# Kernel tuning notes

Measured on AMD Instinct MI355X. Metric: run time of the kernel, lower is better.

Reference implementation:

```python
import jax, jax.numpy as jnp
import numpy as np

B, L, IN_DIM, OUT_DIM, N_BRANCH = 16, 1024, 300, 100, 60

def setup_inputs() -> dict:
    key = jax.random.key(0)
    ks = jax.random.split(key, 7)
    s = 0.05  # weight init scale
    return {
        "x": jax.random.normal(ks[0], (B, L, IN_DIM), dtype=jnp.float32),
        "W2": jax.random.normal(ks[1], (N_BRANCH, OUT_DIM, IN_DIM, 2), dtype=jnp.float32) * s,
        "b2": jax.random.normal(ks[2], (N_BRANCH, OUT_DIM), dtype=jnp.float32) * s,
        "W3": jax.random.normal(ks[3], (N_BRANCH, OUT_DIM, IN_DIM, 3), dtype=jnp.float32) * s,
        "b3": jax.random.normal(ks[4], (N_BRANCH, OUT_DIM), dtype=jnp.float32) * s,
        "W4": jax.random.normal(ks[5], (N_BRANCH, OUT_DIM, IN_DIM, 4), dtype=jnp.float32) * s,
        "b4": jax.random.normal(ks[6], (N_BRANCH, OUT_DIM), dtype=jnp.float32) * s,
    }

def _branch_group(xc, W, b):
    # xc: [B, C, L]; W: [n, o, c, k]; b: [n, o]
    # Batch all n same-kernel-size branches into ONE conv with n*o output channels.
    n, o, c, k = W.shape
    Wf = W.reshape(n * o, c, k)
    y = jax.lax.conv_general_dilated(
        xc, Wf, window_strides=(1,), padding="VALID",
        dimension_numbers=("NCH", "OIH", "NCH"))  # [B, n*o, L-k+1]
    y = jax.nn.relu(y + b.reshape(n * o)[None, :, None])
    y = jnp.max(y, axis=-1)                      # AdaptiveMaxPool1d(1): [B, n*o]
    # concat dim=2 in torch stacks branches along the length axis -> [B, o, n]
    return jnp.transpose(y.reshape(xc.shape[0], n, o), (0, 2, 1))

def reference(x, W2, b2, W3, b3, W4, b4):
    xc = jnp.transpose(x, (0, 2, 1))  # [B, in_dim, L]
    out = jnp.concatenate([
        _branch_group(xc, W2, b2),
        _branch_group(xc, W3, b3),
        _branch_group(xc, W4, b4),
    ], axis=2)                        # [B, out_dim, 180]
    # nn.Dropout(0.5) is identity in eval mode; omitted for the reference baseline.
    return out
```

## Files before the change

### kernel.cpp

```cpp
#include <hip/hip_runtime.h>
#include <cstdint>
#include <cstddef>

typedef unsigned short u16;
typedef unsigned int   u32;
typedef __attribute__((ext_vector_type(8))) short bf16x8;
typedef __attribute__((ext_vector_type(4))) float f32x4;

#define NB   16
#define LL   1024
#define CIN  300
#define CINP 320
#define XPBP (LL*CINP)
#define XELP (NB*XPBP)
#define NCH  6000
#define NCHP 6144
#define ODIM 100

#define BM 256
#define BN 256
#define BK 64

__device__ __forceinline__ u16 f2bf(float f) {
  union { float f; u32 u; } v; v.f = f;
  return (u16)((v.u + 0x7FFFu + ((v.u >> 16) & 1u)) >> 16);
}

typedef __attribute__((address_space(1))) const unsigned int gu32;
typedef __attribute__((address_space(3))) unsigned int lu32;
__device__ __forceinline__ void gload_lds16(const void* g, void* l) {
  __builtin_amdgcn_global_load_lds((gu32*)g, (lu32*)l, 16, 0, 0);
}

#define BAR() asm volatile("s_barrier" ::: "memory")
#define VM2  asm volatile("s_waitcnt vmcnt(2)" ::: "memory")
#define VM0  asm volatile("s_waitcnt vmcnt(0)" ::: "memory")

__global__ void cvt_x_kernel(const float* __restrict__ x, u16* __restrict__ xb) {
  int i8 = (blockIdx.x * 256 + threadIdx.x) * 8;
  int row = i8 / CINP;
  int col = i8 - row * CINP;
  const float* src = x + (size_t)row * CIN + col;
  u16 e[8];
  if (col + 8 <= CIN) {
    float4 a = *(const float4*)src;
    float4 b = *(const float4*)(src + 4);
    e[0]=f2bf(a.x); e[1]=f2bf(a.y); e[2]=f2bf(a.z); e[3]=f2bf(a.w);
    e[4]=f2bf(b.x); e[5]=f2bf(b.y); e[6]=f2bf(b.z); e[7]=f2bf(b.w);
  } else {
    #pragma unroll
    for (int j = 0; j < 8; j++)
      e[j] = (col + j < CIN) ? f2bf(src[j]) : (u16)0;
  }
  uint4 o;
  o.x = (u32)e[0] | ((u32)e[1] << 16);
  o.y = (u32)e[2] | ((u32)e[3] << 16);
  o.z = (u32)e[4] | ((u32)e[5] << 16);
  o.w = (u32)e[6] | ((u32)e[7] << 16);
  *(uint4*)(xb + i8) = o;
}

__global__ void repack_w_kernel(const float* __restrict__ W2, const float* __restrict__ W3,
                                const float* __restrict__ W4, u16* __restrict__ wb) {
  int g = blockIdx.y;
  int kk = g + 2;
  int Kp = kk * CINP;
  int woff = (g == 0) ? 0 : (g == 1) ? NCHP*640 : NCHP*(640+960);
  const float* W = (g == 0) ? W2 : (g == 1) ? W3 : W4;
  int no = blockIdx.x;
  u16* dst = wb + (size_t)woff + (size_t)no * Kp;
  const float* src = W + (size_t)no * (CIN * kk);
  for (int kp = threadIdx.x; kp < Kp; kp += 256) {
    int j = kp / CINP, c = kp - j * CINP;
    u16 v = 0;
    if (no < NCH && c < CIN) v = f2bf(src[c * kk + j]);
    dst[kp] = v;
  }
}

__global__ __launch_bounds__(512, 1)
void gemm_max_kernel(const u16* __restrict__ xb, const u16* __restrict__ wb,
                     const float* __restrict__ b2v, const float* __restrict__ b3v,
                     const float* __restrict__ b4v, float* __restrict__ out) {
  const int id    = blockIdx.x;
  const int g     = 2 - (id / 384);
  const int id2   = id % 384;
  const int b     = id2 / 24;
  const int chblk = id2 % 24;
  const int Kp    = (g + 2) * CINP;
  const int nks   = Kp >> 6;
  const int woff  = (g == 0) ? 0 : (g == 1) ? NCHP*640 : NCHP*(640+960);
  const int Lt    = LL - (g + 2) + 1;

  __shared__ __align__(16) u16 smem[4 * 16384];
  u16* A0s = smem;
  u16* B0s = smem + 16384;
  u16* A1s = smem + 32768;
  u16* B1s = smem + 49152;

  const int tid  = threadIdx.x;
  const int lane = tid & 63;
  const int w    = tid >> 6;
  const int wr   = w >> 2;
  const int wc   = w & 3;

  const u16* __restrict__ xrow = xb + (size_t)b * XPBP;
  const u16* __restrict__ Wg   = wb + (size_t)woff + (size_t)chblk * BN * Kp;

  auto STAGE = [&](const u16* src, int stride, u16* buf, int half) {
    #pragma unroll
    for (int i = 0; i < 2; i++) {
      int c = i * 512 + w * 64 + lane;
      int row128 = c >> 3;
      int colb = ((c & 7) * 16) ^ ((row128 & 7) << 4);
      gload_lds16(src + (size_t)(half * 128 + row128) * stride + (colb >> 1),
                  buf + half * 8192 + i * 4096 + w * 512);
    }
  };

  auto FR = [&](const u16* buf, int grp, int k) -> bf16x8 {
    int row  = grp * 16 + (lane & 15);
    int colb = (k * 64 + ((lane >> 4) << 4)) ^ ((lane & 7) << 4);
    return *(const bf16x8*)(buf + row * 64 + (colb >> 1));
  };

  f32x4 acc[8][4];
  #pragma unroll
  for (int mi = 0; mi < 8; mi++)
    #pragma unroll
    for (int ni = 0; ni < 4; ni++)
      acc[mi][ni] = (f32x4){0.f, 0.f, 0.f, 0.f};

  bf16x8 afrA[4][2];
  bf16x8 afrB[4][2];
  bf16x8 bfr[2][2][2];
  float rmax[4] = { -1e30f, -1e30f, -1e30f, -1e30f };

  auto FOLD = [&](int ttf) {
    #pragma unroll
    for (int mi = 0; mi < 8; mi++) {
      int tb = ttf * 256 + (mi * 2 + wr) * 16 + ((lane >> 4) << 2);
      #pragma unroll
      for (int r = 0; r < 4; r++) {
        bool ok = (tb + r) < Lt;
        #pragma unroll
        for (int ni = 0; ni < 4; ni++)
          if (ok) rmax[ni] = fmaxf(rmax[ni], acc[mi][ni][r]);
      }
      #pragma unroll
      for (int ni = 0; ni < 4; ni++)
        acc[mi][ni] = (f32x4){0.f, 0.f, 0.f, 0.f};
    }
  };

#define READ_A(DST, BUF, MH) do {                                             \
    _Pragma("unroll")                                                         \
    for (int a2 = 0; a2 < 4; a2++) {                                          \
      _Pragma("unroll")                                                       \
      for (int k2 = 0; k2 < 2; k2++)                                          \
        DST[a2][k2] = FR(BUF, ((MH)*4 + a2) * 2 + wr, k2);                    \
    }                                                                         \
  } while (0)

#define READ_B(NH, BUF) do {                                                  \
    _Pragma("unroll")                                                         \
    for (int b2 = 0; b2 < 2; b2++) {                                          \
      _Pragma("unroll")                                                       \
      for (int k2 = 0; k2 < 2; k2++)                                          \
        bfr[NH][b2][k2] = FR(BUF, ((NH)*2 + b2) * 4 + wc, k2);                \
    }                                                                         \
  } while (0)

#define MFMAQ(MH, NH, A) do {                                                 \
    __builtin_amdgcn_s_setprio(1);                                            \
    _Pragma("unroll")                                                         \
    for (int a2 = 0; a2 < 4; a2++)                                            \
      _Pragma("unroll")                                                       \
      for (int b2 = 0; b2 < 2; b2++)                                          \
        _Pragma("unroll")                                                     \
        for (int k2 = 0; k2 < 2; k2++)                                        \
          acc[(MH)*4 + a2][(NH)*2 + b2] =                                     \
            __builtin_amdgcn_mfma_f32_16x16x32_bf16(A[a2][k2],                \
              bfr[NH][b2][k2], acc[(MH)*4 + a2][(NH)*2 + b2], 0, 0, 0);       \
    __builtin_amdgcn_s_setprio(0);                                            \
  } while (0)

  const int NT = 4 * nks;
  int tt = 0, ks = 0;

  STAGE(xrow, CINP, A0s, 0);
  STAGE(Wg,   Kp,   B0s, 0);
  STAGE(Wg,   Kp,   B0s, 1);
  STAGE(xrow, CINP, A0s, 1);
  VM2;
  BAR();
  READ_A(afrA, A0s, 0);
  READ_B(0, B0s);

  for (int s = 0; s < NT - 1; s++) {
    int ks2 = ks + 1, tt2 = tt;
    if (ks2 == nks) { ks2 = 0; tt2++; }
    const u16* sA = xrow + (size_t)tt2 * (256 * CINP) + ks2 * 64;
    const u16* sB = Wg + ks2 * 64;
    u16* cA = (s & 1) ? A1s : A0s;
    u16* cB = (s & 1) ? B1s : B0s;
    u16* nA = (s & 1) ? A0s : A1s;
    u16* nB = (s & 1) ? B0s : B1s;

    STAGE(sA, CINP, nA, 0);
    BAR();
    MFMAQ(0, 0, afrA);
    VM2;
    READ_B(1, cB);
    BAR();
    STAGE(sB, Kp, nB, 0);
    BAR();
    MFMAQ(0, 1, afrA);
    READ_A(afrB, cA, 1);
    BAR();
    STAGE(sB, Kp, nB, 1);
    BAR();
    MFMAQ(1, 0, afrB);
    VM2;
    BAR();
    STAGE(sA, CINP, nA, 1);
    BAR();
    MFMAQ(1, 1, afrB);
    VM2;
    READ_A(afrA, nA, 0);
    READ_B(0, nB);
    BAR();

    if (++ks == nks) { FOLD(tt); ks = 0; tt++; }
  }

  {
    MFMAQ(0, 0, afrA);
    VM0;
    READ_B(1, B1s);
    BAR();
    MFMAQ(0, 1, afrA);
    READ_A(afrB, A1s, 1);
    MFMAQ(1, 0, afrB);
    MFMAQ(1, 1, afrB);
    FOLD(tt);
  }
#undef READ_A
#undef READ_B
#undef MFMAQ

  float cv[4];
  #pragma unroll
  for (int ni = 0; ni < 4; ni++) {
    float v = rmax[ni];
    v = fmaxf(v, __shfl_xor(v, 16));
    v = fmaxf(v, __shfl_xor(v, 32));
    cv[ni] = v;
  }
  __syncthreads();
  float* red = (float*)smem;
  if (lane < 16) {
    #pragma unroll
    for (int ni = 0; ni < 4; ni++)
      red[wr * 256 + (ni * 4 + wc) * 16 + lane] = cv[ni];
  }
  __syncthreads();
  const float* bias = (g == 0) ? b2v : (g == 1) ? b3v : b4v;
  if (tid < 256) {
    float v = fmaxf(red[tid], red[256 + tid]);
    int ch = chblk * BN + tid;
    if (ch < NCH) {
      int n = ch / ODIM, o = ch - n * ODIM;
      out[b * (ODIM * 180) + o * 180 + g * 60 + n] = fmaxf(v + bias[ch], 0.f);
    }
  }
}

extern "C" void kernel_launch(void* const* d_in, const int* in_sizes, int n_in,
                              void* d_out, int out_size, void* d_ws, size_t ws_size,
                              hipStream_t stream) {
  const float* x  = (const float*)d_in[0];
  const float* W2 = (const float*)d_in[1];
  const float* b2 = (const float*)d_in[2];
  const float* W3 = (const float*)d_in[3];
  const float* b3 = (const float*)d_in[4];
  const float* W4 = (const float*)d_in[5];
  const float* b4 = (const float*)d_in[6];
  float* out = (float*)d_out;

  u16* xb = (u16*)d_ws;
  u16* wb = xb + XELP;

  cvt_x_kernel<<<XELP / (256 * 8), 256, 0, stream>>>(x, xb);
  repack_w_kernel<<<dim3(NCHP, 3), 256, 0, stream>>>(W2, W3, W4, wb);
  gemm_max_kernel<<<dim3(1152), 512, 0, stream>>>(xb, wb, b2, b3, b4, out);
}
```

Before: 537.5 us.

## Switch GEMM to 32x32x16 MFMA tiles and merge prep kernels

Replaces the 16x16x32 bf16 MFMA tiling with 32x32x16 MFMA instructions, reorganizing fragment reads, accumulators (f32x16), the max-fold row mapping and the cross-lane reduction. Larger MFMA tiles reduce LDS fragment reads per flop and issue fewer instructions. It also fuses the x conversion and weight repack into a single launch to cut one kernel launch. Register pressure and the fold indexing change, so the row mapping must match the 32x32 output layout.

```diff
diff --git a/kernel.cpp b/kernel.cpp
--- a/kernel.cpp
+++ b/kernel.cpp
@@ -4,8 +4,8 @@
 
 typedef unsigned short u16;
 typedef unsigned int   u32;
-typedef __attribute__((ext_vector_type(8))) short bf16x8;
-typedef __attribute__((ext_vector_type(4))) float f32x4;
+typedef __attribute__((ext_vector_type(8)))  short bf16x8;
+typedef __attribute__((ext_vector_type(16))) float f32x16;
 
 #define NB   16
 #define LL   1024
@@ -36,45 +36,48 @@
 #define VM2  asm volatile("s_waitcnt vmcnt(2)" ::: "memory")
 #define VM0  asm volatile("s_waitcnt vmcnt(0)" ::: "memory")
 
-__global__ void cvt_x_kernel(const float* __restrict__ x, u16* __restrict__ xb) {
-  int i8 = (blockIdx.x * 256 + threadIdx.x) * 8;
-  int row = i8 / CINP;
-  int col = i8 - row * CINP;
-  const float* src = x + (size_t)row * CIN + col;
-  u16 e[8];
-  if (col + 8 <= CIN) {
-    float4 a = *(const float4*)src;
-    float4 b = *(const float4*)(src + 4);
-    e[0]=f2bf(a.x); e[1]=f2bf(a.y); e[2]=f2bf(a.z); e[3]=f2bf(a.w);
-    e[4]=f2bf(b.x); e[5]=f2bf(b.y); e[6]=f2bf(b.z); e[7]=f2bf(b.w);
+__global__ void prep_kernel(const float* __restrict__ x,
+                            const float* __restrict__ W2, const float* __restrict__ W3,
+                            const float* __restrict__ W4,
+                            u16* __restrict__ xb, u16* __restrict__ wb) {
+  int bid = blockIdx.x;
+  if (bid < 3 * NCHP) {
+    int g  = bid / NCHP;
+    int no = bid - g * NCHP;
+    int kk = g + 2;
+    int Kp = kk * CINP;
+    int woff = (g == 0) ? 0 : (g == 1) ? NCHP*640 : NCHP*(640+960);
+    const float* W = (g == 0) ? W2 : (g == 1) ? W3 : W4;
+    u16* dst = wb + (size_t)woff + (size_t)no * Kp;
+    const float* src = W + (size_t)no * (CIN * kk);
+    for (int kp = threadIdx.x; kp < Kp; kp += 256) {
+      int j = kp / CINP, c = kp - j * CINP;
+      u16 v = 0;
+      if (no < NCH && c < CIN) v = f2bf(src[c * kk + j]);
+      dst[kp] = v;
+    }
   } else {
-    #pragma unroll
-    for (int j = 0; j < 8; j++)
-      e[j] = (col + j < CIN) ? f2bf(src[j]) : (u16)0;
-  }
-  uint4 o;
-  o.x = (u32)e[0] | ((u32)e[1] << 16);
-  o.y = (u32)e[2] | ((u32)e[3] << 16);
-  o.z = (u32)e[4] | ((u32)e[5] << 16);
-  o.w = (u32)e[6] | ((u32)e[7] << 16);
-  *(uint4*)(xb + i8) = o;
-}
-
-__global__ void repack_w_kernel(const float* __restrict__ W2, const float* __restrict__ W3,
-                                const float* __restrict__ W4, u16* __restrict__ wb) {
-  int g = blockIdx.y;
-  int kk = g + 2;
-  int Kp = kk * CINP;
-  int woff = (g == 0) ? 0 : (g == 1) ? NCHP*640 : NCHP*(640+960);
-  const float* W = (g == 0) ? W2 : (g == 1) ? W3 : W4;
-  int no = blockIdx.x;
-  u16* dst = wb + (size_t)woff + (size_t)no * Kp;
-  const float* src = W + (size_t)no * (CIN * kk);
-  for (int kp = threadIdx.x; kp < Kp; kp += 256) {
-    int j = kp / CINP, c = kp - j * CINP;
-    u16 v = 0;
-    if (no < NCH && c < CIN) v = f2bf(src[c * kk + j]);
-    dst[kp] = v;
+    int i8 = ((bid - 3 * NCHP) * 256 + threadIdx.x) * 8;
+    int row = i8 / CINP;
+    int col = i8 - row * CINP;
+    const float* src = x + (size_t)row * CIN + col;
+    u16 e[8];
+    if (col + 8 <= CIN) {
+      float4 a = *(const float4*)src;
+      float4 b = *(const float4*)(src + 4);
+      e[0]=f2bf(a.x); e[1]=f2bf(a.y); e[2]=f2bf(a.z); e[3]=f2bf(a.w);
+      e[4]=f2bf(b.x); e[5]=f2bf(b.y); e[6]=f2bf(b.z); e[7]=f2bf(b.w);
+    } else {
+      #pragma unroll
+      for (int j = 0; j < 8; j++)
+        e[j] = (col + j < CIN) ? f2bf(src[j]) : (u16)0;
+    }
+    uint4 o;
+    o.x = (u32)e[0] | ((u32)e[1] << 16);
+    o.y = (u32)e[2] | ((u32)e[3] << 16);
+    o.z = (u32)e[4] | ((u32)e[5] << 16);
+    o.w = (u32)e[6] | ((u32)e[7] << 16);
+    *(uint4*)(xb + i8) = o;
   }
 }
 
@@ -118,70 +121,67 @@
     }
   };
 
-  auto FR = [&](const u16* buf, int grp, int k) -> bf16x8 {
-    int row  = grp * 16 + (lane & 15);
-    int colb = (k * 64 + ((lane >> 4) << 4)) ^ ((lane & 7) << 4);
+  auto FR32 = [&](const u16* buf, int grp, int ksl) -> bf16x8 {
+    int row  = grp * 32 + (lane & 31);
+    int colb = (ksl * 32 + ((lane >> 5) << 4)) ^ ((lane & 7) << 4);
     return *(const bf16x8*)(buf + row * 64 + (colb >> 1));
   };
 
-  f32x4 acc[8][4];
+  f32x16 acc[4][2];
   #pragma unroll
-  for (int mi = 0; mi < 8; mi++)
-    #pragma unroll
-    for (int ni = 0; ni < 4; ni++)
-      acc[mi][ni] = (f32x4){0.f, 0.f, 0.f, 0.f};
-
-  bf16x8 afrA[4][2];
-  bf16x8 afrB[4][2];
-  bf16x8 bfr[2][2][2];
-  float rmax[4] = { -1e30f, -1e30f, -1e30f, -1e30f };
+  for (int a2 = 0; a2 < 4; a2++)
+    #pragma unroll
+    for (int b2 = 0; b2 < 2; b2++)
+      #pragma unroll
+      for (int q = 0; q < 16; q++)
+        acc[a2][b2][q] = 0.f;
+
+  bf16x8 afrA[2][4];
+  bf16x8 afrB[2][4];
+  bf16x8 bfr[2][4];
+  float rmax[2] = { -1e30f, -1e30f };
 
   auto FOLD = [&](int ttf) {
     #pragma unroll
-    for (int mi = 0; mi < 8; mi++) {
-      int tb = ttf * 256 + (mi * 2 + wr) * 16 + ((lane >> 4) << 2);
+    for (int a2 = 0; a2 < 4; a2++) {
+      int rowbase = ttf * 256 + (a2 * 2 + wr) * 32 + ((lane >> 5) << 2);
       #pragma unroll
-      for (int r = 0; r < 4; r++) {
-        bool ok = (tb + r) < Lt;
+      for (int r = 0; r < 16; r++) {
+        int t = rowbase + (r & 3) + 8 * (r >> 2);
+        bool ok = t < Lt;
         #pragma unroll
-        for (int ni = 0; ni < 4; ni++)
-          if (ok) rmax[ni] = fmaxf(rmax[ni], acc[mi][ni][r]);
+        for (int b2 = 0; b2 < 2; b2++) {
+          if (ok) rmax[b2] = fmaxf(rmax[b2], acc[a2][b2][r]);
+          acc[a2][b2][r] = 0.f;
+        }
       }
-      #pragma unroll
-      for (int ni = 0; ni < 4; ni++)
-        acc[mi][ni] = (f32x4){0.f, 0.f, 0.f, 0.f};
     }
   };
 
-#define READ_A(DST, BUF, MH) do {                                             \
+#define READ_A32(DST, BUF, MH) do {                                           \
     _Pragma("unroll")                                                         \
-    for (int a2 = 0; a2 < 4; a2++) {                                          \
+    for (int a2l = 0; a2l < 2; a2l++) {                                       \
       _Pragma("unroll")                                                       \
-      for (int k2 = 0; k2 < 2; k2++)                                          \
-        DST[a2][k2] = FR(BUF, ((MH)*4 + a2) * 2 + wr, k2);                    \
+      for (int ksl = 0; ksl < 4; ksl++)                                       \
+        DST[a2l][ksl] = FR32(BUF, ((MH)*2 + a2l) * 2 + wr, ksl);              \
     }                                                                         \
   } while (0)
 
-#define READ_B(NH, BUF) do {                                                  \
+#define READ_B32(NH, BUF) do {                                                \
     _Pragma("unroll")                                                         \
-    for (int b2 = 0; b2 < 2; b2++) {                                          \
-      _Pragma("unroll")                                                       \
-      for (int k2 = 0; k2 < 2; k2++)                                          \
-        bfr[NH][b2][k2] = FR(BUF, ((NH)*2 + b2) * 4 + wc, k2);                \
-    }                                                                         \
+    for (int ksl = 0; ksl < 4; ksl++)                                         \
+      bfr[NH][ksl] = FR32(BUF, (NH)*4 + wc, ksl);                             \
   } while (0)
 
-#define MFMAQ(MH, NH, A) do {                                                 \
+#define MFMAQ32(MH, NH, A) do {                                               \
     __builtin_amdgcn_s_setprio(1);                                            \
     _Pragma("unroll")                                                         \
-    for (int a2 = 0; a2 < 4; a2++)                                            \
+    for (int ksl = 0; ksl < 4; ksl++)                                         \
       _Pragma("unroll")                                                       \
-      for (int b2 = 0; b2 < 2; b2++)                                          \
-        _Pragma("unroll")                                                     \
-        for (int k2 = 0; k2 < 2; k2++)                                        \
-          acc[(MH)*4 + a2][(NH)*2 + b2] =                                     \
-            __builtin_amdgcn_mfma_f32_16x16x32_bf16(A[a2][k2],                \
-              bfr[NH][b2][k2], acc[(MH)*4 + a2][(NH)*2 + b2], 0, 0, 0);       \
+      for (int a2l = 0; a2l < 2; a2l++)                                       \
+        acc[(MH)*2 + a2l][NH] =                                               \
+          __builtin_amdgcn_mfma_f32_32x32x16_bf16(A[a2l][ksl],                \
+            bfr[NH][ksl], acc[(MH)*2 + a2l][NH], 0, 0, 0);                    \
     __builtin_amdgcn_s_setprio(0);                                            \
   } while (0)
 
@@ -194,8 +194,8 @@
   STAGE(xrow, CINP, A0s, 1);
   VM2;
   BAR();
-  READ_A(afrA, A0s, 0);
-  READ_B(0, B0s);
+  READ_A32(afrA, A0s, 0);
+  READ_B32(0, B0s);
 
   for (int s = 0; s < NT - 1; s++) {
     int ks2 = ks + 1, tt2 = tt;
@@ -209,60 +209,59 @@
 
     STAGE(sA, CINP, nA, 0);
     BAR();
-    MFMAQ(0, 0, afrA);
+    MFMAQ32(0, 0, afrA);
     VM2;
-    READ_B(1, cB);
+    READ_B32(1, cB);
     BAR();
     STAGE(sB, Kp, nB, 0);
     BAR();
-    MFMAQ(0, 1, afrA);
-    READ_A(afrB, cA, 1);
+    MFMAQ32(0, 1, afrA);
+    READ_A32(afrB, cA, 1);
     BAR();
     STAGE(sB, Kp, nB, 1);
     BAR();
-    MFMAQ(1, 0, afrB);
+    MFMAQ32(1, 0, afrB);
     VM2;
     BAR();
     STAGE(sA, CINP, nA, 1);
     BAR();
-    MFMAQ(1, 1, afrB);
+    MFMAQ32(1, 1, afrB);
     VM2;
-    READ_A(afrA, nA, 0);
-    READ_B(0, nB);
+    READ_A32(afrA, nA, 0);
+    READ_B32(0, nB);
     BAR();
 
     if (++ks == nks) { FOLD(tt); ks = 0; tt++; }
   }
 
   {
-    MFMAQ(0, 0, afrA);
+    MFMAQ32(0, 0, afrA);
     VM0;
-    READ_B(1, B1s);
-    BAR();
-    MFMAQ(0, 1, afrA);
-    READ_A(afrB, A1s, 1);
-    MFMAQ(1, 0, afrB);
-    MFMAQ(1, 1, afrB);
+    READ_B32(1, B1s);
+    BAR();
+    MFMAQ32(0, 1, afrA);
+    READ_A32(afrB, A1s, 1);
+    MFMAQ32(1, 0, afrB);
+    MFMAQ32(1, 1, afrB);
     FOLD(tt);
   }
-#undef READ_A
-#undef READ_B
-#undef MFMAQ
-
-  float cv[4];
+#undef READ_A32
+#undef READ_B32
+#undef MFMAQ32
+
+  float cv[2];
   #pragma unroll
-  for (int ni = 0; ni < 4; ni++) {
-    float v = rmax[ni];
-    v = fmaxf(v, __shfl_xor(v, 16));
+  for (int b2 = 0; b2 < 2; b2++) {
+    float v = rmax[b2];
     v = fmaxf(v, __shfl_xor(v, 32));
-    cv[ni] = v;
+    cv[b2] = v;
   }
   __syncthreads();
   float* red = (float*)smem;
-  if (lane < 16) {
-    #pragma unroll
-    for (int ni = 0; ni < 4; ni++)
-      red[wr * 256 + (ni * 4 + wc) * 16 + lane] = cv[ni];
+  if (lane < 32) {
+    #pragma unroll
+    for (int b2 = 0; b2 < 2; b2++)
+      red[wr * 256 + (b2 * 4 + wc) * 32 + lane] = cv[b2];
   }
   __syncthreads();
   const float* bias = (g == 0) ? b2v : (g == 1) ? b3v : b4v;
@@ -291,7 +290,6 @@
   u16* xb = (u16*)d_ws;
   u16* wb = xb + XELP;
 
-  cvt_x_kernel<<<XELP / (256 * 8), 256, 0, stream>>>(x, xb);
-  repack_w_kernel<<<dim3(NCHP, 3), 256, 0, stream>>>(W2, W3, W4, wb);
+  prep_kernel<<<3 * NCHP + XELP / (256 * 8), 256, 0, stream>>>(x, W2, W3, W4, xb, wb);
   gemm_max_kernel<<<dim3(1152), 512, 0, stream>>>(xb, wb, b2, b3, b4, out);
 }
```

Result: slower. 578.8 us (+7.7%).

## Use a persistent balanced GEMM schedule with half-length segments and atomicMax merge

Applied to the files above, without the earlier changes.

The GEMM launch becomes a persistent grid of 256 blocks, one per CU. Each block walks nine segments spread across the three kernel sizes, and each segment covers half the sequence length for one batch and channel block. The software pipeline now runs continuously across segment boundaries, so the tail imbalance from 1152 unequal blocks should go away. Partial maxima are merged with atomicMax on float bits, which is only valid because ReLU outputs are non-negative and the output is zeroed first. The x conversion, the weight repack and the output zeroing are fused into a single prep launch.

```diff
diff --git a/kernel.cpp b/kernel.cpp
--- a/kernel.cpp
+++ b/kernel.cpp
@@ -16,6 +16,8 @@
 #define NCH  6000
 #define NCHP 6144
 #define ODIM 100
+#define OUTN (NB*ODIM*180)
+#define TOTSTEPS 270
 
 #define BM 256
 #define BN 256
@@ -36,45 +38,56 @@
 #define VM2  asm volatile("s_waitcnt vmcnt(2)" ::: "memory")
 #define VM0  asm volatile("s_waitcnt vmcnt(0)" ::: "memory")
 
-__global__ void cvt_x_kernel(const float* __restrict__ x, u16* __restrict__ xb) {
-  int i8 = (blockIdx.x * 256 + threadIdx.x) * 8;
-  int row = i8 / CINP;
-  int col = i8 - row * CINP;
-  const float* src = x + (size_t)row * CIN + col;
-  u16 e[8];
-  if (col + 8 <= CIN) {
-    float4 a = *(const float4*)src;
-    float4 b = *(const float4*)(src + 4);
-    e[0]=f2bf(a.x); e[1]=f2bf(a.y); e[2]=f2bf(a.z); e[3]=f2bf(a.w);
-    e[4]=f2bf(b.x); e[5]=f2bf(b.y); e[6]=f2bf(b.z); e[7]=f2bf(b.w);
+__global__ void prep_kernel(const float* __restrict__ x,
+                            const float* __restrict__ W2, const float* __restrict__ W3,
+                            const float* __restrict__ W4,
+                            u16* __restrict__ xb, u16* __restrict__ wb,
+                            float* __restrict__ out) {
+  int bid = blockIdx.x;
+  if (bid < 141) {
+    int i8 = (bid * 256 + threadIdx.x) * 8;
+    if (i8 < OUTN) {
+      *(float4*)(out + i8)     = make_float4(0.f, 0.f, 0.f, 0.f);
+      *(float4*)(out + i8 + 4) = make_float4(0.f, 0.f, 0.f, 0.f);
+    }
+  } else if (bid < 141 + 3 * NCHP) {
+    int wbid = bid - 141;
+    int g  = wbid / NCHP;
+    int no = wbid - g * NCHP;
+    int kk = g + 2;
+    int Kp = kk * CINP;
+    int woff = (g == 0) ? 0 : (g == 1) ? NCHP*640 : NCHP*(640+960);
+    const float* W = (g == 0) ? W2 : (g == 1) ? W3 : W4;
+    u16* dst = wb + (size_t)woff + (size_t)no * Kp;
+    const float* src = W + (size_t)no * (CIN * kk);
+    for (int kp = threadIdx.x; kp < Kp; kp += 256) {
+      int j = kp / CINP, c = kp - j * CINP;
+      u16 v = 0;
+      if (no < NCH && c < CIN) v = f2bf(src[c * kk + j]);
+      dst[kp] = v;
+    }
   } else {
-    #pragma unroll
-    for (int j = 0; j < 8; j++)
-      e[j] = (col + j < CIN) ? f2bf(src[j]) : (u16)0;
-  }
-  uint4 o;
-  o.x = (u32)e[0] | ((u32)e[1] << 16);
-  o.y = (u32)e[2] | ((u32)e[3] << 16);
-  o.z = (u32)e[4] | ((u32)e[5] << 16);
-  o.w = (u32)e[6] | ((u32)e[7] << 16);
-  *(uint4*)(xb + i8) = o;
-}
-
-__global__ void repack_w_kernel(const float* __restrict__ W2, const float* __restrict__ W3,
-                                const float* __restrict__ W4, u16* __restrict__ wb) {
-  int g = blockIdx.y;
-  int kk = g + 2;
-  int Kp = kk * CINP;
-  int woff = (g == 0) ? 0 : (g == 1) ? NCHP*640 : NCHP*(640+960);
-  const float* W = (g == 0) ? W2 : (g == 1) ? W3 : W4;
-  int no = blockIdx.x;
-  u16* dst = wb + (size_t)woff + (size_t)no * Kp;
-  const float* src = W + (size_t)no * (CIN * kk);
-  for (int kp = threadIdx.x; kp < Kp; kp += 256) {
-    int j = kp / CINP, c = kp - j * CINP;
-    u16 v = 0;
-    if (no < NCH && c < CIN) v = f2bf(src[c * kk + j]);
-    dst[kp] = v;
+    int i8 = ((bid - 141 - 3 * NCHP) * 256 + threadIdx.x) * 8;
+    int row = i8 / CINP;
+    int col = i8 - row * CINP;
+    const float* src = x + (size_t)row * CIN + col;
+    u16 e[8];
+    if (col + 8 <= CIN) {
+      float4 a = *(const float4*)src;
+      float4 b = *(const float4*)(src + 4);
+      e[0]=f2bf(a.x); e[1]=f2bf(a.y); e[2]=f2bf(a.z); e[3]=f2bf(a.w);
+      e[4]=f2bf(b.x); e[5]=f2bf(b.y); e[6]=f2bf(b.z); e[7]=f2bf(b.w);
+    } else {
+      #pragma unroll
+      for (int j = 0; j < 8; j++)
+        e[j] = (col + j < CIN) ? f2bf(src[j]) : (u16)0;
+    }
+    uint4 o;
+    o.x = (u32)e[0] | ((u32)e[1] << 16);
+    o.y = (u32)e[2] | ((u32)e[3] << 16);
+    o.z = (u32)e[4] | ((u32)e[5] << 16);
+    o.w = (u32)e[6] | ((u32)e[7] << 16);
+    *(uint4*)(xb + i8) = o;
   }
 }
 
@@ -82,17 +95,10 @@
 void gemm_max_kernel(const u16* __restrict__ xb, const u16* __restrict__ wb,
                      const float* __restrict__ b2v, const float* __restrict__ b3v,
                      const float* __restrict__ b4v, float* __restrict__ out) {
-  const int id    = blockIdx.x;
-  const int g     = 2 - (id / 384);
-  const int id2   = id % 384;
-  const int b     = id2 / 24;
-  const int chblk = id2 % 24;
-  const int Kp    = (g + 2) * CINP;
-  const int nks   = Kp >> 6;
-  const int woff  = (g == 0) ? 0 : (g == 1) ? NCHP*640 : NCHP*(640+960);
-  const int Lt    = LL - (g + 2) + 1;
+  const int cu = blockIdx.x;
 
   __shared__ __align__(16) u16 smem[4 * 16384];
+  __shared__ float scratch[512];
   u16* A0s = smem;
   u16* B0s = smem + 16384;
   u16* A1s = smem + 32768;
@@ -104,8 +110,26 @@
   const int wr   = w >> 2;
   const int wc   = w & 3;
 
-  const u16* __restrict__ xrow = xb + (size_t)b * XPBP;
-  const u16* __restrict__ Wg   = wb + (size_t)woff + (size_t)chblk * BN * Kp;
+  auto segdec = [&](int seg, int& g, int& bb, int& cb, int& tp) {
+    g = (seg < 3) ? 2 : (seg < 6) ? 1 : 0;
+    int hu = cu * 3 + (seg - (2 - g) * 3);
+    bb = hu / 48; int r = hu - bb * 48; cb = r >> 1; tp = r & 1;
+  };
+
+  int sc_seg = 0, sc_tile = 0, sc_ks = 0;
+  auto stgaddr = [&](const u16*& sA, const u16*& sB, int& sKp) {
+    int g, bb, cb, tp; segdec(sc_seg, g, bb, cb, tp);
+    int Kp = (g + 2) * CINP;
+    int woff = (g == 0) ? 0 : (g == 1) ? NCHP*640 : NCHP*(640+960);
+    sA = xb + (size_t)bb * XPBP + (size_t)(tp * 2 + sc_tile) * (256 * CINP) + sc_ks * 64;
+    sB = wb + (size_t)woff + (size_t)cb * BN * Kp + sc_ks * 64;
+    sKp = Kp;
+  };
+  auto adv = [&]() {
+    int g = (sc_seg < 3) ? 2 : (sc_seg < 6) ? 1 : 0;
+    int nks = (g + 2) * 5;
+    if (++sc_ks == nks) { sc_ks = 0; if (++sc_tile == 2) { sc_tile = 0; ++sc_seg; } }
+  };
 
   auto STAGE = [&](const u16* src, int stride, u16* buf, int half) {
     #pragma unroll
@@ -135,23 +159,6 @@
   bf16x8 afrB[4][2];
   bf16x8 bfr[2][2][2];
   float rmax[4] = { -1e30f, -1e30f, -1e30f, -1e30f };
-
-  auto FOLD = [&](int ttf) {
-    #pragma unroll
-    for (int mi = 0; mi < 8; mi++) {
-      int tb = ttf * 256 + (mi * 2 + wr) * 16 + ((lane >> 4) << 2);
-      #pragma unroll
-      for (int r = 0; r < 4; r++) {
-        bool ok = (tb + r) < Lt;
-        #pragma unroll
-        for (int ni = 0; ni < 4; ni++)
-          if (ok) rmax[ni] = fmaxf(rmax[ni], acc[mi][ni][r]);
-      }
-      #pragma unroll
-      for (int ni = 0; ni < 4; ni++)
-        acc[mi][ni] = (f32x4){0.f, 0.f, 0.f, 0.f};
-    }
-  };
 
 #define READ_A(DST, BUF, MH) do {                                             \
     _Pragma("unroll")                                                         \
@@ -185,95 +192,126 @@
     __builtin_amdgcn_s_setprio(0);                                            \
   } while (0)
 
-  const int NT = 4 * nks;
-  int tt = 0, ks = 0;
-
-  STAGE(xrow, CINP, A0s, 0);
-  STAGE(Wg,   Kp,   B0s, 0);
-  STAGE(Wg,   Kp,   B0s, 1);
-  STAGE(xrow, CINP, A0s, 1);
+  {
+    const u16 *sA, *sB; int sKp;
+    stgaddr(sA, sB, sKp);
+    STAGE(sA, CINP, A0s, 0);
+    STAGE(sB, sKp, B0s, 0);
+    STAGE(sB, sKp, B0s, 1);
+    STAGE(sA, CINP, A0s, 1);
+    adv();
+  }
   VM2;
   BAR();
   READ_A(afrA, A0s, 0);
   READ_B(0, B0s);
 
-  for (int s = 0; s < NT - 1; s++) {
-    int ks2 = ks + 1, tt2 = tt;
-    if (ks2 == nks) { ks2 = 0; tt2++; }
-    const u16* sA = xrow + (size_t)tt2 * (256 * CINP) + ks2 * 64;
-    const u16* sB = Wg + ks2 * 64;
-    u16* cA = (s & 1) ? A1s : A0s;
-    u16* cB = (s & 1) ? B1s : B0s;
-    u16* nA = (s & 1) ? A0s : A1s;
-    u16* nB = (s & 1) ? B0s : B1s;
-
-    STAGE(sA, CINP, nA, 0);
-    BAR();
-    MFMAQ(0, 0, afrA);
-    VM2;
-    READ_B(1, cB);
-    BAR();
-    STAGE(sB, Kp, nB, 0);
-    BAR();
-    MFMAQ(0, 1, afrA);
-    READ_A(afrB, cA, 1);
-    BAR();
-    STAGE(sB, Kp, nB, 1);
-    BAR();
-    MFMAQ(1, 0, afrB);
-    VM2;
-    BAR();
-    STAGE(sA, CINP, nA, 1);
-    BAR();
-    MFMAQ(1, 1, afrB);
-    VM2;
-    READ_A(afrA, nA, 0);
-    READ_B(0, nB);
-    BAR();
-
-    if (++ks == nks) { FOLD(tt); ks = 0; tt++; }
-  }
-
-  {
-    MFMAQ(0, 0, afrA);
-    VM0;
-    READ_B(1, B1s);
-    BAR();
-    MFMAQ(0, 1, afrA);
-    READ_A(afrB, A1s, 1);
-    MFMAQ(1, 0, afrB);
-    MFMAQ(1, 1, afrB);
-    FOLD(tt);
+  int step = 0;
+  for (int seg = 0; seg < 9; seg++) {
+    int g, bb, cb, tp; segdec(seg, g, bb, cb, tp);
+    const int nks = (g + 2) * 5;
+    const int Lt  = LL - (g + 2) + 1;
+
+    for (int tile = 0; tile < 2; tile++) {
+      for (int ks = 0; ks < nks; ks++, step++) {
+        u16* cA = (step & 1) ? A1s : A0s;
+        u16* cB = (step & 1) ? B1s : B0s;
+        u16* nA = (step & 1) ? A0s : A1s;
+        u16* nB = (step & 1) ? B0s : B1s;
+
+        if (step < TOTSTEPS - 1) {
+          const u16 *sA, *sB; int sKp;
+          stgaddr(sA, sB, sKp);
+          adv();
+          STAGE(sA, CINP, nA, 0);
+          BAR();
+          MFMAQ(0, 0, afrA);
+          VM2;
+          READ_B(1, cB);
+          BAR();
+          STAGE(sB, sKp, nB, 0);
+          BAR();
+          MFMAQ(0, 1, afrA);
+          READ_A(afrB, cA, 1);
+          BAR();
+          STAGE(sB, sKp, nB, 1);
+          BAR();
+          MFMAQ(1, 0, afrB);
+          VM2;
+          BAR();
+          STAGE(sA, CINP, nA, 1);
+          BAR();
+          MFMAQ(1, 1, afrB);
+          VM2;
+          READ_A(afrA, nA, 0);
+          READ_B(0, nB);
+          BAR();
+        } else {
+          MFMAQ(0, 0, afrA);
+          VM0;
+          READ_B(1, cB);
+          BAR();
+          MFMAQ(0, 1, afrA);
+          READ_A(afrB, cA, 1);
+          MFMAQ(1, 0, afrB);
+          MFMAQ(1, 1, afrB);
+        }
+      }
+
+      {
+        int ttabs = tp * 2 + tile;
+        #pragma unroll
+        for (int mi = 0; mi < 8; mi++) {
+          int tb = ttabs * 256 + (mi * 2 + wr) * 16 + ((lane >> 4) << 2);
+          #pragma unroll
+          for (int r = 0; r < 4; r++) {
+            bool ok = (tb + r) < Lt;
+            #pragma unroll
+            for (int ni = 0; ni < 4; ni++)
+              if (ok) rmax[ni] = fmaxf(rmax[ni], acc[mi][ni][r]);
+          }
+          #pragma unroll
+          for (int ni = 0; ni < 4; ni++)
+            acc[mi][ni] = (f32x4){0.f, 0.f, 0.f, 0.f};
+        }
+      }
+    }
+
+    {
+      float cv[4];
+      #pragma unroll
+      for (int ni = 0; ni < 4; ni++) {
+        float v = rmax[ni];
+        v = fmaxf(v, __shfl_xor(v, 16));
+        v = fmaxf(v, __shfl_xor(v, 32));
+        cv[ni] = v;
+        rmax[ni] = -1e30f;
+      }
+      if (lane < 16) {
+        #pragma unroll
+        for (int ni = 0; ni < 4; ni++)
+          scratch[wr * 256 + (ni * 4 + wc) * 16 + lane] = cv[ni];
+      }
+      asm volatile("s_waitcnt lgkmcnt(0)" ::: "memory");
+      BAR();
+      const float* bias = (g == 0) ? b2v : (g == 1) ? b3v : b4v;
+      if (tid < 256) {
+        float v = fmaxf(scratch[tid], scratch[256 + tid]);
+        int ch = cb * BN + tid;
+        if (ch < NCH) {
+          int n = ch / ODIM, o = ch - n * ODIM;
+          float r = fmaxf(v + bias[ch], 0.f);
+          atomicMax((u32*)&out[bb * (ODIM * 180) + o * 180 + g * 60 + n],
+                    __float_as_uint(r));
+        }
+      }
+      asm volatile("s_waitcnt lgkmcnt(0)" ::: "memory");
+      BAR();
+    }
   }
 #undef READ_A
 #undef READ_B
 #undef MFMAQ
-
-  float cv[4];
-  #pragma unroll
-  for (int ni = 0; ni < 4; ni++) {
-    float v = rmax[ni];
-    v = fmaxf(v, __shfl_xor(v, 16));
-    v = fmaxf(v, __shfl_xor(v, 32));
-    cv[ni] = v;
-  }
-  __syncthreads();
-  float* red = (float*)smem;
-  if (lane < 16) {
-    #pragma unroll
-    for (int ni = 0; ni < 4; ni++)
-      red[wr * 256 + (ni * 4 + wc) * 16 + lane] = cv[ni];
-  }
-  __syncthreads();
-  const float* bias = (g == 0) ? b2v : (g == 1) ? b3v : b4v;
-  if (tid < 256) {
-    float v = fmaxf(red[tid], red[256 + tid]);
-    int ch = chblk * BN + tid;
-    if (ch < NCH) {
-      int n = ch / ODIM, o = ch - n * ODIM;
-      out[b * (ODIM * 180) + o * 180 + g * 60 + n] = fmaxf(v + bias[ch], 0.f);
-    }
-  }
 }
 
 extern "C" void kernel_launch(void* const* d_in, const int* in_sizes, int n_in,
@@ -291,7 +329,7 @@
   u16* xb = (u16*)d_ws;
   u16* wb = xb + XELP;
 
-  cvt_x_kernel<<<XELP / (256 * 8), 256, 0, stream>>>(x, xb);
-  repack_w_kernel<<<dim3(NCHP, 3), 256, 0, stream>>>(W2, W3, W4, wb);
-  gemm_max_kernel<<<dim3(1152), 512, 0, stream>>>(xb, wb, b2, b3, b4, out);
-}
+  prep_kernel<<<141 + 3 * NCHP + XELP / (256 * 8), 256, 0, stream>>>(
+      x, W2, W3, W4, xb, wb, out);
+  gemm_max_kernel<<<dim3(256), 512, 0, stream>>>(xb, wb, b2, b3, b4, out);
+}
```

After: 892.0 us. 1.66x slower.
